# Optimization experiments

Measured on AMD Instinct MI355X. Metric: run time of the kernel, lower is better.

Reference implementation:

```python
import jax, jax.numpy as jnp
import numpy as np

N = 50000          # nodes
E = 400000         # edges
MUL0 = 16          # multiplicity of 0e irreps (node & message)
MUL1 = 8           # multiplicity of 1o irreps
RBF = 8
HID = 64
CUTOFF = 5.0
WNUM = MUL0*MUL0 + MUL1*MUL0 + MUL0*MUL1 + MUL1*MUL1  # 576 tp weights per edge
EPS = 1e-8
INV_SQRT3 = 1.0 / np.sqrt(3.0).astype(np.float32)
A_PATH = 1.0 / np.sqrt(float(MUL0 + MUL1))  # e3nn path normalization (fan_in = 24 for both outputs)


def _split_sv(x):
    # x: [n, 40] -> scalars [n,16], vectors [n,8,3]
    return x[:, :MUL0], x[:, MUL0:].reshape(-1, MUL1, 3)


def _irrep_norm(x):
    # RMS-normalize each irrep block separately (IrrepNorm)
    s, v = _split_sv(x)
    s_rms = jnp.sqrt(jnp.mean(s * s, axis=-1, keepdims=True) + EPS)
    v_rms = jnp.sqrt(jnp.mean(jnp.sum(v * v, axis=-1), axis=-1, keepdims=True) + EPS)
    return jnp.concatenate([s / s_rms, (v / v_rms[:, :, None]).reshape(-1, MUL1 * 3)], axis=-1)


def setup_inputs() -> dict:
    key = jax.random.key(0)
    ks = jax.random.split(key, 20)
    inp = {
        'x': jax.random.normal(ks[0], (N, MUL0 + 3 * MUL1), jnp.float32),
        'edge_src': jax.random.randint(ks[1], (E,), 0, N, jnp.int32),
        'edge_dst': jax.random.randint(ks[2], (E,), 0, N, jnp.int32),
        'edge_sh': jax.random.normal(ks[3], (E, 4), jnp.float32),
        'edge_rbf': jax.random.uniform(ks[4], (E, RBF), jnp.float32),
        'edge_len': jax.random.uniform(ks[5], (E,), jnp.float32) * CUTOFF,
        # radial MLP producing per-edge TP weights
        'w_r1': jax.random.normal(ks[6], (RBF, HID), jnp.float32) / np.sqrt(RBF),
        'b_r1': jnp.zeros((HID,), jnp.float32),
        'w_r2': jax.random.normal(ks[7], (HID, WNUM), jnp.float32) / np.sqrt(HID),
        'b_r2': jnp.zeros((WNUM,), jnp.float32),
        # edge gate MLP
        'w_g1': jax.random.normal(ks[8], (RBF, HID), jnp.float32) / np.sqrt(RBF),
        'b_g1': jnp.zeros((HID,), jnp.float32),
        'w_g2': jax.random.normal(ks[9], (HID, 1), jnp.float32) / np.sqrt(HID),
        'b_g2': jnp.zeros((1,), jnp.float32),
        # msg_linear: 16x0e+8x1o -> (16x0e scalars + 8x0e gates) + 8x1o gated
        'Wm_s': jax.random.normal(ks[10], (MUL0, MUL0 + MUL1), jnp.float32),
        'Wm_v': jax.random.normal(ks[11], (MUL1, MUL1), jnp.float32),
        # update_linear and self_linear: 16x0e+8x1o -> 16x0e+8x1o
        'Wu_s': jax.random.normal(ks[12], (MUL0, MUL0), jnp.float32),
        'Wu_v': jax.random.normal(ks[13], (MUL1, MUL1), jnp.float32),
        'Ws_s': jax.random.normal(ks[14], (MUL0, MUL0), jnp.float32),
        'Ws_v': jax.random.normal(ks[15], (MUL1, MUL1), jnp.float32),
        'res_scale': jnp.asarray(0.1, jnp.float32),
    }
    return inp


def reference(x, edge_src, edge_dst, edge_sh, edge_rbf, edge_len,
              w_r1, b_r1, w_r2, b_r2, w_g1, b_g1, w_g2, b_g2,
              Wm_s, Wm_v, Wu_s, Wu_v, Ws_s, Ws_v, res_scale):
    x_norm = _irrep_norm(x)
    xs, xv = _split_sv(x_norm)

    # per-edge TP weights from radial MLP
    w = jax.nn.silu(edge_rbf @ w_r1 + b_r1) @ w_r2 + b_r2            # [E, 576]
    o = MUL0 * MUL0
    w1 = w[:, :o].reshape(-1, MUL0, MUL0)                            # 0e x 0e -> 0e
    w2 = w[:, o:o + MUL1 * MUL0].reshape(-1, MUL1, MUL0)             # 1o x 1o -> 0e
    o += MUL1 * MUL0
    w3 = w[:, o:o + MUL0 * MUL1].reshape(-1, MUL0, MUL1)             # 0e x 1o -> 1o
    o += MUL0 * MUL1
    w4 = w[:, o:].reshape(-1, MUL1, MUL1)                            # 1o x 0e -> 1o

    # gather per-edge source features
    s_e = xs[edge_src]                                               # [E,16]
    v_e = xv[edge_src]                                               # [E,8,3]
    sh0 = edge_sh[:, :1]                                             # [E,1]
    sh1 = edge_sh[:, 1:4]                                            # [E,3]

    # fully-connected tensor product (CG for l<=1, component norm, path norm)
    m0 = A_PATH * (jnp.einsum('ei,eij->ej', s_e * sh0, w1)
                   + INV_SQRT3 * jnp.einsum('eic,ec,eij->ej', v_e, sh1, w2))   # [E,16]
    m1 = A_PATH * (jnp.einsum('ei,eij,ec->ejc', s_e, w3, sh1)
                   + jnp.einsum('eic,eij->ejc', v_e * sh0[:, :, None], w4))    # [E,8,3]

    # cutoff and sigmoid edge gate
    cw = 0.5 * (jnp.cos(jnp.pi * edge_len / CUTOFF) + 1.0) * (edge_len < CUTOFF)
    gw = jax.nn.sigmoid(jax.nn.silu(edge_rbf @ w_g1 + b_g1) @ w_g2 + b_g2)     # [E,1]
    ew = cw[:, None] * gw                                                      # [E,1]
    m0 = m0 * ew
    m1 = m1 * ew[:, :, None]

    # scatter-add into destination nodes, normalize by total edge weight
    agg0 = jax.ops.segment_sum(m0, edge_dst, num_segments=N)                   # [N,16]
    agg1 = jax.ops.segment_sum(m1.reshape(-1, MUL1 * 3), edge_dst, num_segments=N).reshape(-1, MUL1, 3)
    norm = jax.ops.segment_sum(ew, edge_dst, num_segments=N)                   # [N,1]
    norm = jnp.maximum(norm, EPS)
    agg0 = agg0 / norm
    agg1 = agg1 / norm[:, :, None]

    # msg_linear (equivariant linear, fan-in normalized)
    sc = agg0 @ Wm_s / np.sqrt(MUL0)                                           # [N,24]
    vv = jnp.einsum('nic,ij->njc', agg1, Wm_v) / np.sqrt(MUL1)                 # [N,8,3]

    # gated nonlinearity
    scal = jax.nn.silu(sc[:, :MUL0])
    gates = jax.nn.sigmoid(sc[:, MUL0:])
    vg = vv * gates[:, :, None]

    # update + self interaction, residual
    out_s = scal @ Wu_s / np.sqrt(MUL0) + xs @ Ws_s / np.sqrt(MUL0)
    out_v = (jnp.einsum('nic,ij->njc', vg, Wu_v) + jnp.einsum('nic,ij->njc', xv, Ws_v)) / np.sqrt(MUL1)
    out = jnp.concatenate([out_s, out_v.reshape(-1, MUL1 * 3)], axis=-1)
    return x + res_scale * out
```

## Files before the change

### kernel.cpp

```cpp
#include <hip/hip_runtime.h>
#include <cstdint>

#define MUL0 16
#define MUL1 8
#define NRBF 8
#define HID 64
#define WNUM 576
#define CUTOFF 5.0f
#define EPSF 1e-8f

#define INV_SQRT3 0.57735026918962576f
#define A_PATH    0.20412414523193154f
#define Q16       0.25f
#define Q8        0.35355339059327373f
#define PI_OVER_CUT 0.62831853071795865f

typedef _Float16 f16;
typedef _Float16 f16x8 __attribute__((ext_vector_type(8)));
typedef float f32x4 __attribute__((ext_vector_type(4)));

#define MFMA16(a, b, cc) __builtin_amdgcn_mfma_f32_16x16x32_f16(a, b, cc, 0, 0, 0)

__device__ __forceinline__ float sigm(float x) { return 1.0f / (1.0f + __expf(-x)); }

typedef __attribute__((address_space(1))) const unsigned char* gptr_t;
typedef __attribute__((address_space(3))) unsigned char* lptr_t;

__device__ __forceinline__ void stage16(const void* g, void* l) {
  __builtin_amdgcn_global_load_lds((gptr_t)g, (lptr_t)l, 16, 0, 0);
}

extern "C" __global__ __launch_bounds__(256) void k_prep_w2t(
    const float* __restrict__ w_r2, f16* __restrict__ W2T,
    int* __restrict__ hist, int N) {
  int t = blockIdx.x * 256 + threadIdx.x;
  if (t < HID * WNUM) {
    int n = t >> 6, k = t & 63;
    int jt = n >> 4, cc = n & 15;
    int h = k >> 3, e = k & 7;
    int dst = jt * 1024 + cc * 64 + ((h ^ (cc & 7)) << 3) + e;
    W2T[dst] = (f16)w_r2[k * WNUM + n];
  }
  if (t < N) hist[t] = 0;
}

extern "C" __global__ __launch_bounds__(64) void k_xnorm(
    const float* __restrict__ x, float* __restrict__ xnorm,
    float* __restrict__ agg0, float* __restrict__ agg1,
    float* __restrict__ normb, int N) {
  int n = blockIdx.x * 64 + threadIdx.x;
  if (n >= N) return;
  const float4* xr = (const float4*)(x + (long long)n * 40);
  float4 vv[10];
#pragma unroll
  for (int i = 0; i < 10; i++) vv[i] = xr[i];
  float* f = (float*)vv;
  float ss = 0.f, vs = 0.f;
#pragma unroll
  for (int i = 0; i < 16; i++) ss += f[i] * f[i];
#pragma unroll
  for (int i = 16; i < 40; i++) vs += f[i] * f[i];
  float sr = rsqrtf(ss * (1.0f / 16.0f) + EPSF);
  float vr = rsqrtf(vs * (1.0f / 8.0f) + EPSF);
#pragma unroll
  for (int i = 0; i < 16; i++) f[i] *= sr;
#pragma unroll
  for (int i = 16; i < 40; i++) f[i] *= vr;
  float4* o = (float4*)(xnorm + (long long)n * 40);
#pragma unroll
  for (int i = 0; i < 10; i++) o[i] = vv[i];
  float4 z = {0.f, 0.f, 0.f, 0.f};
  float4* pa0 = (float4*)(agg0 + (long long)n * 16);
#pragma unroll
  for (int i = 0; i < 4; i++) pa0[i] = z;
  float4* pa1 = (float4*)(agg1 + (long long)n * 24);
#pragma unroll
  for (int i = 0; i < 6; i++) pa1[i] = z;
  normb[n] = 0.f;
}

extern "C" __global__ __launch_bounds__(256) void k_hist(
    const int* __restrict__ edst, int* __restrict__ hist, int E) {
  int e = blockIdx.x * 256 + threadIdx.x;
  if (e < E) atomicAdd(&hist[edst[e]], 1);
}

extern "C" __global__ __launch_bounds__(256) void k_scan1(
    const int* __restrict__ hist, int* __restrict__ iscan,
    int* __restrict__ bsum, int N) {
  __shared__ int sm[256];
  int i = blockIdx.x * 256 + threadIdx.x;
  int t = threadIdx.x;
  sm[t] = (i < N) ? hist[i] : 0;
  __syncthreads();
#pragma unroll
  for (int d = 1; d < 256; d <<= 1) {
    int add = (t >= d) ? sm[t - d] : 0;
    __syncthreads();
    sm[t] += add;
    __syncthreads();
  }
  if (i < N) iscan[i] = sm[t];
  if (t == 255) bsum[blockIdx.x] = sm[255];
}

extern "C" __global__ __launch_bounds__(256) void k_scan2(
    int* __restrict__ bsum, int nb) {
  __shared__ int sm[256];
  int t = threadIdx.x;
  sm[t] = (t < nb) ? bsum[t] : 0;
  __syncthreads();
#pragma unroll
  for (int d = 1; d < 256; d <<= 1) {
    int add = (t >= d) ? sm[t - d] : 0;
    __syncthreads();
    sm[t] += add;
    __syncthreads();
  }
  if (t < nb) bsum[t] = sm[t];
}

extern "C" __global__ __launch_bounds__(256) void k_scan3(
    const int* __restrict__ hist, const int* __restrict__ iscan,
    const int* __restrict__ bsum, int* __restrict__ cursor, int N) {
  int i = blockIdx.x * 256 + threadIdx.x;
  if (i >= N) return;
  int base = blockIdx.x ? bsum[blockIdx.x - 1] : 0;
  cursor[i] = iscan[i] - hist[i] + base;
}

extern "C" __global__ __launch_bounds__(256) void k_scatter(
    const int* __restrict__ edst, int* __restrict__ cursor,
    int* __restrict__ perm, int E) {
  int e = blockIdx.x * 256 + threadIdx.x;
  if (e >= E) return;
  int p = atomicAdd(&cursor[edst[e]], 1);
  perm[p] = e;
}

extern "C" __global__ __launch_bounds__(256, 3) void k_edge(
    const float* __restrict__ xnorm, const int* __restrict__ perm,
    const int* __restrict__ esrc, const int* __restrict__ edst,
    const float* __restrict__ sh, const float* __restrict__ rbf,
    const float* __restrict__ elen,
    const float* __restrict__ w_r1, const float* __restrict__ b_r1,
    const float* __restrict__ w_g1, const float* __restrict__ b_g1,
    const float* __restrict__ w_g2, const float* __restrict__ b_g2,
    const float* __restrict__ b_r2, const f16* __restrict__ W2T,
    float* __restrict__ agg0, float* __restrict__ agg1,
    float* __restrict__ normb, int E) {
  __shared__ __align__(16) char smem[53248];
  f16   (*s_H)[32][72]  = (f16(*)[32][72])(smem);
  float (*s_sn)[32][20] = (float(*)[32][20])(smem + 18432);
  float (*s_v)[32][26]  = (float(*)[32][26])(smem + 28672);
  float (*s_a1)[32][10] = (float(*)[32][10])(smem + 41984);
  float (*s_sh)[32][4]  = (float(*)[32][4])(smem + 47104);
  float (*s_rbf)[32][8] = (float(*)[32][8])(smem + 49152);
  float* s_bias = (float*)(smem + 49152);

  const int t = threadIdx.x;
  const int w = t >> 6;
  const int lane = t & 63;
  const long long eb = (long long)blockIdx.x * 128 + w * 32;

  int pl = 0, dstv = 0, srcv = 0;
  float lenv = 1e9f;
  if (lane < 32) {
    long long g2 = eb + lane;
    if (g2 < E) pl = perm[g2];
    srcv = esrc[pl];
    dstv = edst[pl];
    lenv = elen[pl];
    *(float4*)&s_sh[w][lane][0] = *(const float4*)&sh[(long long)pl * 4];
  }
  {
    int e = lane >> 1, half = lane & 1;
    int pe = __shfl(pl, e);
    *(float4*)&s_rbf[w][e][half * 4] =
        *(const float4*)&rbf[(long long)pe * 8 + half * 4];
  }
  __syncthreads();

  {
    const int ge_l = lane >> 2;
    const int part = lane & 3;
#pragma unroll
    for (int g = 0; g < 2; g++) {
      int e = g * 16 + ge_l;
      int srcn = __shfl(srcv, e);
      const float* xr = xnorm + (long long)srcn * 40;
      if (part < 2) {
        float4 aLo = *(const float4*)(xr + part * 8);
        float4 aHi = *(const float4*)(xr + part * 8 + 4);
        *(float4*)&s_sn[w][e][part * 8] = aLo;
        *(float4*)&s_sn[w][e][part * 8 + 4] = aHi;
      } else {
        const int i0 = (part - 2) * 4;
        const float* vp = xr + 16 + i0 * 3;
        float4 v0 = *(const float4*)(vp);
        float4 v1 = *(const float4*)(vp + 4);
        float4 v2 = *(const float4*)(vp + 8);
        *(float4*)&s_v[w][e][i0 * 3] = v0;
        *(float4*)&s_v[w][e][i0 * 3 + 4] = v1;
        *(float4*)&s_v[w][e][i0 * 3 + 8] = v2;
        float4 shq = *(const float4*)&s_sh[w][e][0];
        float s1x = shq.y, s1y = shq.z, s1z = shq.w;
        s_a1[w][e][i0]     = INV_SQRT3 * (v0.x * s1x + v0.y * s1y + v0.z * s1z);
        s_a1[w][e][i0 + 1] = INV_SQRT3 * (v0.w * s1x + v1.x * s1y + v1.y * s1z);
        s_a1[w][e][i0 + 2] = INV_SQRT3 * (v1.z * s1x + v1.w * s1y + v2.x * s1z);
        s_a1[w][e][i0 + 3] = INV_SQRT3 * (v2.y * s1x + v2.z * s1y + v2.w * s1z);
      }
    }
  }

  {
    float wr[8];
#pragma unroll
    for (int r = 0; r < 8; r++) wr[r] = w_r1[r * HID + lane];
    float bh = b_r1[lane];
#pragma unroll 4
    for (int u = 0; u < 32; u++) {
      float4 ra = *(const float4*)&s_rbf[w][u][0];
      float4 rb2 = *(const float4*)&s_rbf[w][u][4];
      float acc = bh + ra.x * wr[0] + ra.y * wr[1] + ra.z * wr[2] + ra.w * wr[3]
                     + rb2.x * wr[4] + rb2.y * wr[5] + rb2.z * wr[6] + rb2.w * wr[7];
      s_H[w][u][lane] = (f16)(acc * sigm(acc));
    }
  }

  float ewv = 0.f;
  {
    const int eg = lane & 31;
    const int hf = lane >> 5;
    float4 ga = *(const float4*)&s_rbf[w][eg][0];
    float4 gb = *(const float4*)&s_rbf[w][eg][4];
    float rv[8] = {ga.x, ga.y, ga.z, ga.w, gb.x, gb.y, gb.z, gb.w};
    float accp = 0.f;
#pragma unroll
    for (int ch = 0; ch < 2; ch++) {
      const int base = hf * 32 + ch * 16;
      float ttv[16];
      {
        const float4 b0 = *(const float4*)&b_g1[base];
        const float4 b1 = *(const float4*)&b_g1[base + 4];
        const float4 b2 = *(const float4*)&b_g1[base + 8];
        const float4 b3 = *(const float4*)&b_g1[base + 12];
        ttv[0] = b0.x; ttv[1] = b0.y; ttv[2] = b0.z; ttv[3] = b0.w;
        ttv[4] = b1.x; ttv[5] = b1.y; ttv[6] = b1.z; ttv[7] = b1.w;
        ttv[8] = b2.x; ttv[9] = b2.y; ttv[10] = b2.z; ttv[11] = b2.w;
        ttv[12] = b3.x; ttv[13] = b3.y; ttv[14] = b3.z; ttv[15] = b3.w;
      }
#pragma unroll
      for (int r = 0; r < 8; r++) {
        const float* wg = w_g1 + r * HID + base;
        float4 w0 = *(const float4*)(wg);
        float4 w1 = *(const float4*)(wg + 4);
        float4 w2 = *(const float4*)(wg + 8);
        float4 w3 = *(const float4*)(wg + 12);
        float rr = rv[r];
        ttv[0] += rr * w0.x; ttv[1] += rr * w0.y; ttv[2] += rr * w0.z; ttv[3] += rr * w0.w;
        ttv[4] += rr * w1.x; ttv[5] += rr * w1.y; ttv[6] += rr * w1.z; ttv[7] += rr * w1.w;
        ttv[8] += rr * w2.x; ttv[9] += rr * w2.y; ttv[10] += rr * w2.z; ttv[11] += rr * w2.w;
        ttv[12] += rr * w3.x; ttv[13] += rr * w3.y; ttv[14] += rr * w3.z; ttv[15] += rr * w3.w;
      }
      const float4 g0 = *(const float4*)&w_g2[base];
      const float4 g1 = *(const float4*)&w_g2[base + 4];
      const float4 g2 = *(const float4*)&w_g2[base + 8];
      const float4 g3 = *(const float4*)&w_g2[base + 12];
      float gw[16] = {g0.x, g0.y, g0.z, g0.w, g1.x, g1.y, g1.z, g1.w,
                      g2.x, g2.y, g2.z, g2.w, g3.x, g3.y, g3.z, g3.w};
#pragma unroll
      for (int k = 0; k < 16; k++) accp += ttv[k] * sigm(ttv[k]) * gw[k];
    }
    accp += __shfl_xor(accp, 32);
    if (lane < 32) {
      long long g2e = eb + lane;
      if (g2e < E) {
        float cw = (lenv < CUTOFF) ? 0.5f * (__cosf(PI_OVER_CUT * lenv) + 1.0f) : 0.f;
        ewv = cw * sigm(accp + b_g2[0]);
      }
    }
  }
  __syncthreads();

  const int quad = lane >> 4;
  const int c = lane & 15;

  const f16x8 af00 = *(const f16x8*)&s_H[w][c][quad * 8];
  const f16x8 af01 = *(const f16x8*)&s_H[w][c][32 + quad * 8];
  const f16x8 af10 = *(const f16x8*)&s_H[w][16 + c][quad * 8];
  const f16x8 af11 = *(const f16x8*)&s_H[w][16 + c][32 + quad * 8];
  for (int i = t; i < WNUM; i += 256) s_bias[i] = b_r2[i];
  __syncthreads();

  char* ring = smem;
  const char* W2Tc = (const char*)W2T;
  const int lofs = w * 1024;
  const int gofs = w * 1024 + lane * 16;

  stage16(W2Tc + gofs, ring + lofs);

  const int rd0 = c * 128 + ((quad ^ (c & 7)) << 4);
  const int rd1 = c * 128 + (((quad + 4) ^ (c & 7)) << 4);

  float p1[2][4] = {{0.f}}, p2[2][4] = {{0.f}}, t3[2][4] = {{0.f}};
  float mx[2][4] = {{0.f}}, my[2][4] = {{0.f}}, mz[2][4] = {{0.f}};

#pragma unroll 1
  for (int ch = 0; ch < 8; ch++) {
    __syncthreads();
    stage16(W2Tc + (ch + 1) * 4096 + gofs, ring + ((ch + 1) & 1) * 4096 + lofs);
    const char* bb = ring + (ch & 1) * 4096;
#pragma unroll
    for (int hf2 = 0; hf2 < 2; hf2++) {
      const int jt = ch * 2 + hf2;
      const char* tb = bb + hf2 * 2048;
      f16x8 b0 = *(const f16x8*)(tb + rd0);
      f16x8 b1 = *(const f16x8*)(tb + rd1);
      float bias = s_bias[jt * 16 + c];
      f32x4 C0 = {0.f, 0.f, 0.f, 0.f};
      C0 = MFMA16(af00, b0, C0); C0 = MFMA16(af01, b1, C0);
      f32x4 C1 = {0.f, 0.f, 0.f, 0.f};
      C1 = MFMA16(af10, b0, C1); C1 = MFMA16(af11, b1, C1);
#pragma unroll
      for (int r = 0; r < 4; r++) {
        p1[0][r] += s_sn[w][quad * 4 + r][jt] * (C0[r] + bias);
        p1[1][r] += s_sn[w][16 + quad * 4 + r][jt] * (C1[r] + bias);
      }
    }
  }
#pragma unroll 1
  for (int ch = 8; ch < 12; ch++) {
    __syncthreads();
    stage16(W2Tc + (ch + 1) * 4096 + gofs, ring + ((ch + 1) & 1) * 4096 + lofs);
    const char* bb = ring + (ch & 1) * 4096;
#pragma unroll
    for (int hf2 = 0; hf2 < 2; hf2++) {
      const int jt = ch * 2 + hf2;
      const char* tb = bb + hf2 * 2048;
      f16x8 b0 = *(const f16x8*)(tb + rd0);
      f16x8 b1 = *(const f16x8*)(tb + rd1);
      float bias = s_bias[jt * 16 + c];
      f32x4 C0 = {0.f, 0.f, 0.f, 0.f};
      C0 = MFMA16(af00, b0, C0); C0 = MFMA16(af01, b1, C0);
      f32x4 C1 = {0.f, 0.f, 0.f, 0.f};
      C1 = MFMA16(af10, b0, C1); C1 = MFMA16(af11, b1, C1);
      const int i = jt - 16;
#pragma unroll
      for (int r = 0; r < 4; r++) {
        p2[0][r] += s_a1[w][quad * 4 + r][i] * (C0[r] + bias);
        p2[1][r] += s_a1[w][16 + quad * 4 + r][i] * (C1[r] + bias);
      }
    }
  }
#pragma unroll 1
  for (int ch = 12; ch < 16; ch++) {
    __syncthreads();
    stage16(W2Tc + (ch + 1) * 4096 + gofs, ring + ((ch + 1) & 1) * 4096 + lofs);
    const char* bb = ring + (ch & 1) * 4096;
#pragma unroll
    for (int hf2 = 0; hf2 < 2; hf2++) {
      const int jt = ch * 2 + hf2;
      const char* tb = bb + hf2 * 2048;
      f16x8 b0 = *(const f16x8*)(tb + rd0);
      f16x8 b1 = *(const f16x8*)(tb + rd1);
      float bias = s_bias[jt * 16 + c];
      f32x4 C0 = {0.f, 0.f, 0.f, 0.f};
      C0 = MFMA16(af00, b0, C0); C0 = MFMA16(af01, b1, C0);
      f32x4 C1 = {0.f, 0.f, 0.f, 0.f};
      C1 = MFMA16(af10, b0, C1); C1 = MFMA16(af11, b1, C1);
      const int i = (jt - 24) * 2 + (c >> 3);
#pragma unroll
      for (int r = 0; r < 4; r++) {
        t3[0][r] += s_sn[w][quad * 4 + r][i] * (C0[r] + bias);
        t3[1][r] += s_sn[w][16 + quad * 4 + r][i] * (C1[r] + bias);
      }
    }
  }
#pragma unroll 1
  for (int ch = 16; ch < 18; ch++) {
    __syncthreads();
    if (ch < 17)
      stage16(W2Tc + (ch + 1) * 4096 + gofs, ring + ((ch + 1) & 1) * 4096 + lofs);
    const char* bb = ring + (ch & 1) * 4096;
#pragma unroll
    for (int hf2 = 0; hf2 < 2; hf2++) {
      const int jt = ch * 2 + hf2;
      const char* tb = bb + hf2 * 2048;
      f16x8 b0 = *(const f16x8*)(tb + rd0);
      f16x8 b1 = *(const f16x8*)(tb + rd1);
      float bias = s_bias[jt * 16 + c];
      f32x4 C0 = {0.f, 0.f, 0.f, 0.f};
      C0 = MFMA16(af00, b0, C0); C0 = MFMA16(af01, b1, C0);
      f32x4 C1 = {0.f, 0.f, 0.f, 0.f};
      C1 = MFMA16(af10, b0, C1); C1 = MFMA16(af11, b1, C1);
      const int i = (jt - 32) * 2 + (c >> 3);
#pragma unroll
      for (int r = 0; r < 4; r++) {
        float wv0 = C0[r] + bias;
        float wv1 = C1[r] + bias;
        mx[0][r] += s_v[w][quad * 4 + r][3 * i] * wv0;
        my[0][r] += s_v[w][quad * 4 + r][3 * i + 1] * wv0;
        mz[0][r] += s_v[w][quad * 4 + r][3 * i + 2] * wv0;
        mx[1][r] += s_v[w][16 + quad * 4 + r][3 * i] * wv1;
        my[1][r] += s_v[w][16 + quad * 4 + r][3 * i + 1] * wv1;
        mz[1][r] += s_v[w][16 + quad * 4 + r][3 * i + 2] * wv1;
      }
    }
  }

#pragma unroll
  for (int g = 0; g < 2; g++)
#pragma unroll
    for (int r = 0; r < 4; r++) {
      t3[g][r] += __shfl_xor(t3[g][r], 8);
      mx[g][r] += __shfl_xor(mx[g][r], 8);
      my[g][r] += __shfl_xor(my[g][r], 8);
      mz[g][r] += __shfl_xor(mz[g][r], 8);
    }

#pragma unroll
  for (int g = 0; g < 2; g++) {
    const int e0g = g * 16 + quad * 4;
    int cur = __shfl(dstv, e0g);
    float acc0 = 0.f, a1x = 0.f, a1y = 0.f, a1z = 0.f, nacc = 0.f;
#pragma unroll
    for (int r = 0; r < 4; r++) {
      const int e = e0g + r;
      const int dst = __shfl(dstv, e);
      const float ew = __shfl(ewv, e);
      if (dst != cur) {
        atomicAdd(&agg0[(long long)cur * 16 + c], acc0);
        if (c < 8) {
          long long b = (long long)cur * 24 + (long long)c * 3;
          atomicAdd(&agg1[b], a1x);
          atomicAdd(&agg1[b + 1], a1y);
          atomicAdd(&agg1[b + 2], a1z);
        } else if (c == 8) {
          atomicAdd(&normb[cur], nacc);
        }
        acc0 = a1x = a1y = a1z = nacc = 0.f;
        cur = dst;
      }
      float sc2 = A_PATH * ew;
      float sh0 = s_sh[w][e][0];
      acc0 += (sh0 * p1[g][r] + p2[g][r]) * sc2;
      if (c < 8) {
        float t3v = t3[g][r] * sc2;
        float scs = sc2 * sh0;
        a1x += t3v * s_sh[w][e][1] + mx[g][r] * scs;
        a1y += t3v * s_sh[w][e][2] + my[g][r] * scs;
        a1z += t3v * s_sh[w][e][3] + mz[g][r] * scs;
      } else if (c == 8) {
        nacc += ew;
      }
    }
    atomicAdd(&agg0[(long long)cur * 16 + c], acc0);
    if (c < 8) {
      long long b = (long long)cur * 24 + (long long)c * 3;
      atomicAdd(&agg1[b], a1x);
      atomicAdd(&agg1[b + 1], a1y);
      atomicAdd(&agg1[b + 2], a1z);
    } else if (c == 8) {
      atomicAdd(&normb[cur], nacc);
    }
  }
}

extern "C" __global__ __launch_bounds__(64) void k_node(
    const float* __restrict__ x, const float* __restrict__ xnorm,
    const float* __restrict__ agg0, const float* __restrict__ agg1,
    const float* __restrict__ normb, const float* __restrict__ Wm_s,
    const float* __restrict__ Wm_v, const float* __restrict__ Wu_s,
    const float* __restrict__ Wu_v, const float* __restrict__ Ws_s,
    const float* __restrict__ Ws_v, const float* __restrict__ res_scale_p,
    float* __restrict__ out, int N) {
  __shared__ float sWms[384];
  __shared__ float sWmv[64];
  __shared__ float sWus[256];
  __shared__ float sWuv[64];
  __shared__ float sWss[256];
  __shared__ float sWsv[64];
  int t = threadIdx.x;
  for (int i = t; i < 384; i += 64) sWms[i] = Wm_s[i];
  sWmv[t] = Wm_v[t];
  for (int i = t; i < 256; i += 64) sWus[i] = Wu_s[i];
  sWuv[t] = Wu_v[t];
  for (int i = t; i < 256; i += 64) sWss[i] = Ws_s[i];
  sWsv[t] = Ws_v[t];
  __syncthreads();
  int n = blockIdx.x * 64 + t;
  if (n >= N) return;

  float inv = 1.0f / fmaxf(normb[n], EPSF);
  float4 a04[4], a14[6];
  {
    const float4* p = (const float4*)(agg0 + (long long)n * 16);
#pragma unroll
    for (int i = 0; i < 4; i++) a04[i] = p[i];
    const float4* q = (const float4*)(agg1 + (long long)n * 24);
#pragma unroll
    for (int i = 0; i < 6; i++) a14[i] = q[i];
  }
  float* a0 = (float*)a04;
  float* a1 = (float*)a14;
#pragma unroll
  for (int i = 0; i < 16; i++) a0[i] *= inv;
#pragma unroll
  for (int i = 0; i < 24; i++) a1[i] *= inv;

  float scal[16], gate[8];
#pragma unroll
  for (int jj = 0; jj < 24; jj++) {
    float acc = 0.f;
#pragma unroll
    for (int i = 0; i < 16; i++) acc += a0[i] * sWms[i * 24 + jj];
    acc *= Q16;
    if (jj < 16) scal[jj] = acc * sigm(acc);
    else gate[jj - 16] = sigm(acc);
  }
  float vg[24];
#pragma unroll
  for (int j = 0; j < 8; j++) {
    float g = gate[j];
#pragma unroll
    for (int cc = 0; cc < 3; cc++) {
      float acc = 0.f;
#pragma unroll
      for (int i = 0; i < 8; i++) acc += a1[i * 3 + cc] * sWmv[i * 8 + j];
      vg[j * 3 + cc] = acc * Q8 * g;
    }
  }
  float4 xn4[10], xo4[10];
  {
    const float4* p = (const float4*)(xnorm + (long long)n * 40);
    const float4* q = (const float4*)(x + (long long)n * 40);
#pragma unroll
    for (int i = 0; i < 10; i++) { xn4[i] = p[i]; xo4[i] = q[i]; }
  }
  const float* xn = (const float*)xn4;
  const float* xo = (const float*)xo4;
  float rs = res_scale_p[0];

  float4 ob[10];
  float* ov = (float*)ob;
#pragma unroll
  for (int j = 0; j < 16; j++) {
    float acc = 0.f, acc2 = 0.f;
#pragma unroll
    for (int i = 0; i < 16; i++) {
      acc += scal[i] * sWus[i * 16 + j];
      acc2 += xn[i] * sWss[i * 16 + j];
    }
    ov[j] = xo[j] + rs * ((acc + acc2) * Q16);
  }
#pragma unroll
  for (int j = 0; j < 8; j++) {
#pragma unroll
    for (int cc = 0; cc < 3; cc++) {
      float acc = 0.f;
#pragma unroll
      for (int i = 0; i < 8; i++)
        acc += vg[i * 3 + cc] * sWuv[i * 8 + j] + xn[16 + i * 3 + cc] * sWsv[i * 8 + j];
      ov[16 + j * 3 + cc] = xo[16 + j * 3 + cc] + rs * (acc * Q8);
    }
  }
  float4* po = (float4*)(out + (long long)n * 40);
#pragma unroll
  for (int i = 0; i < 10; i++) po[i] = ob[i];
}

extern "C" void kernel_launch(void* const* d_in, const int* in_sizes, int n_in,
                              void* d_out, int out_size, void* d_ws, size_t ws_size,
                              hipStream_t stream) {
  const float* x = (const float*)d_in[0];
  const int* esrc = (const int*)d_in[1];
  const int* edst = (const int*)d_in[2];
  const float* sh = (const float*)d_in[3];
  const float* rbf = (const float*)d_in[4];
  const float* elen = (const float*)d_in[5];
  const float* w_r1 = (const float*)d_in[6];
  const float* b_r1 = (const float*)d_in[7];
  const float* w_r2 = (const float*)d_in[8];
  const float* b_r2 = (const float*)d_in[9];
  const float* w_g1 = (const float*)d_in[10];
  const float* b_g1 = (const float*)d_in[11];
  const float* w_g2 = (const float*)d_in[12];
  const float* b_g2 = (const float*)d_in[13];
  const float* Wm_s = (const float*)d_in[14];
  const float* Wm_v = (const float*)d_in[15];
  const float* Wu_s = (const float*)d_in[16];
  const float* Wu_v = (const float*)d_in[17];
  const float* Ws_s = (const float*)d_in[18];
  const float* Ws_v = (const float*)d_in[19];
  const float* res_scale = (const float*)d_in[20];

  const int N = in_sizes[0] / 40;
  const int E = in_sizes[1];

  char* ws = (char*)d_ws;
  size_t off = 0;
  float* xnorm = (float*)(ws + off); off += (size_t)N * 40 * sizeof(float);
  off = (off + 255) & ~(size_t)255;
  float* agg0 = (float*)(ws + off); off += (size_t)N * 16 * sizeof(float);
  float* agg1 = (float*)(ws + off); off += (size_t)N * 24 * sizeof(float);
  float* normb = (float*)(ws + off); off += (size_t)N * sizeof(float);
  off = (off + 255) & ~(size_t)255;
  f16* W2T = (f16*)(ws + off); off += (size_t)WNUM * 64 * sizeof(f16);
  off = (off + 255) & ~(size_t)255;
  int* hist   = (int*)(ws + off); off += (size_t)N * sizeof(int);
  int* iscan  = (int*)(ws + off); off += (size_t)N * sizeof(int);
  int* cursor = (int*)(ws + off); off += (size_t)N * sizeof(int);
  int* bsum   = (int*)(ws + off); off += 256 * sizeof(int);
  off = (off + 255) & ~(size_t)255;
  int* perm   = (int*)(ws + off); off += (size_t)E * sizeof(int);

  const int nbE = (E + 255) / 256;
  const int nbN = (N + 255) / 256;

  k_prep_w2t<<<nbN, 256, 0, stream>>>(w_r2, W2T, hist, N);
  k_hist<<<nbE, 256, 0, stream>>>(edst, hist, E);
  k_scan1<<<nbN, 256, 0, stream>>>(hist, iscan, bsum, N);
  k_scan2<<<1, 256, 0, stream>>>(bsum, nbN);
  k_scan3<<<nbN, 256, 0, stream>>>(hist, iscan, bsum, cursor, N);
  k_scatter<<<nbE, 256, 0, stream>>>(edst, cursor, perm, E);

  k_xnorm<<<(N + 63) / 64, 64, 0, stream>>>(x, xnorm, agg0, agg1, normb, N);

  int nblk = (E + 127) / 128;
  k_edge<<<nblk, 256, 0, stream>>>(xnorm, perm, esrc, edst, sh, rbf, elen,
                                   w_r1, b_r1, w_g1, b_g1, w_g2, b_g2, b_r2,
                                   W2T, agg0, agg1, normb, E);

  k_node<<<(N + 63) / 64, 64, 0, stream>>>(x, xnorm, agg0, agg1, normb, Wm_s,
                                           Wm_v, Wu_s, Wu_v, Ws_s, Ws_v,
                                           res_scale, (float*)d_out, N);
}
```

Baseline: 336.8 us.

## Fuse preprocessing kernels, use single-pass decoupled scan, deepen W2T staging chunks

Merges weight transpose, histogram, and node normalization/zeroing into one kernel and replaces the three-kernel block scan with a single-pass scan, where each block publishes its total and spin-waits on the totals of earlier blocks. The aim is to cut kernel launch count and idle gaps between the small setup kernels. The edge kernel now stages W2T in 8KB chunks of four tiles instead of 4KB chunks of two, halving the number of barriers per edge block. The spin-wait relies on earlier blocks being resident, and the larger staging ring uses more LDS, which could lower occupancy.

```diff
diff --git a/kernel.cpp b/kernel.cpp
--- a/kernel.cpp
+++ b/kernel.cpp
@@ -30,68 +30,65 @@
   __builtin_amdgcn_global_load_lds((gptr_t)g, (lptr_t)l, 16, 0, 0);
 }
 
-extern "C" __global__ __launch_bounds__(256) void k_prep_w2t(
-    const float* __restrict__ w_r2, f16* __restrict__ W2T,
-    int* __restrict__ hist, int N) {
-  int t = blockIdx.x * 256 + threadIdx.x;
-  if (t < HID * WNUM) {
-    int n = t >> 6, k = t & 63;
+extern "C" __global__ __launch_bounds__(256) void k_pre(
+    const float* __restrict__ x, float* __restrict__ xnorm,
+    float* __restrict__ agg0, float* __restrict__ agg1,
+    float* __restrict__ normb, const float* __restrict__ w_r2,
+    f16* __restrict__ W2T, const int* __restrict__ edst,
+    int* __restrict__ hist, int N, int E) {
+  long long gid = (long long)blockIdx.x * 256 + threadIdx.x;
+
+  if (gid < HID * WNUM) {
+    int n = (int)gid >> 6, k = (int)gid & 63;
     int jt = n >> 4, cc = n & 15;
     int h = k >> 3, e = k & 7;
     int dst = jt * 1024 + cc * 64 + ((h ^ (cc & 7)) << 3) + e;
     W2T[dst] = (f16)w_r2[k * WNUM + n];
   }
-  if (t < N) hist[t] = 0;
+
+  if (gid < E) atomicAdd(&hist[edst[gid]], 1);
+
+  if (gid < N) {
+    long long n = gid;
+    const float4* xr = (const float4*)(x + n * 40);
+    float4 vv[10];
+#pragma unroll
+    for (int i = 0; i < 10; i++) vv[i] = xr[i];
+    float* f = (float*)vv;
+    float ss = 0.f, vs = 0.f;
+#pragma unroll
+    for (int i = 0; i < 16; i++) ss += f[i] * f[i];
+#pragma unroll
+    for (int i = 16; i < 40; i++) vs += f[i] * f[i];
+    float sr = rsqrtf(ss * (1.0f / 16.0f) + EPSF);
+    float vr = rsqrtf(vs * (1.0f / 8.0f) + EPSF);
+#pragma unroll
+    for (int i = 0; i < 16; i++) f[i] *= sr;
+#pragma unroll
+    for (int i = 16; i < 40; i++) f[i] *= vr;
+    float4* o = (float4*)(xnorm + n * 40);
+#pragma unroll
+    for (int i = 0; i < 10; i++) o[i] = vv[i];
+    float4 z = {0.f, 0.f, 0.f, 0.f};
+    float4* pa0 = (float4*)(agg0 + n * 16);
+#pragma unroll
+    for (int i = 0; i < 4; i++) pa0[i] = z;
+    float4* pa1 = (float4*)(agg1 + n * 24);
+#pragma unroll
+    for (int i = 0; i < 6; i++) pa1[i] = z;
+    normb[n] = 0.f;
+  }
 }
 
-extern "C" __global__ __launch_bounds__(64) void k_xnorm(
-    const float* __restrict__ x, float* __restrict__ xnorm,
-    float* __restrict__ agg0, float* __restrict__ agg1,
-    float* __restrict__ normb, int N) {
-  int n = blockIdx.x * 64 + threadIdx.x;
-  if (n >= N) return;
-  const float4* xr = (const float4*)(x + (long long)n * 40);
-  float4 vv[10];
-#pragma unroll
-  for (int i = 0; i < 10; i++) vv[i] = xr[i];
-  float* f = (float*)vv;
-  float ss = 0.f, vs = 0.f;
-#pragma unroll
-  for (int i = 0; i < 16; i++) ss += f[i] * f[i];
-#pragma unroll
-  for (int i = 16; i < 40; i++) vs += f[i] * f[i];
-  float sr = rsqrtf(ss * (1.0f / 16.0f) + EPSF);
-  float vr = rsqrtf(vs * (1.0f / 8.0f) + EPSF);
-#pragma unroll
-  for (int i = 0; i < 16; i++) f[i] *= sr;
-#pragma unroll
-  for (int i = 16; i < 40; i++) f[i] *= vr;
-  float4* o = (float4*)(xnorm + (long long)n * 40);
-#pragma unroll
-  for (int i = 0; i < 10; i++) o[i] = vv[i];
-  float4 z = {0.f, 0.f, 0.f, 0.f};
-  float4* pa0 = (float4*)(agg0 + (long long)n * 16);
-#pragma unroll
-  for (int i = 0; i < 4; i++) pa0[i] = z;
-  float4* pa1 = (float4*)(agg1 + (long long)n * 24);
-#pragma unroll
-  for (int i = 0; i < 6; i++) pa1[i] = z;
-  normb[n] = 0.f;
-}
-
-extern "C" __global__ __launch_bounds__(256) void k_hist(
-    const int* __restrict__ edst, int* __restrict__ hist, int E) {
-  int e = blockIdx.x * 256 + threadIdx.x;
-  if (e < E) atomicAdd(&hist[edst[e]], 1);
-}
-
-extern "C" __global__ __launch_bounds__(256) void k_scan1(
-    const int* __restrict__ hist, int* __restrict__ iscan,
-    int* __restrict__ bsum, int N) {
+extern "C" __global__ __launch_bounds__(256) void k_scan(
+    const int* __restrict__ hist, int* __restrict__ cursor,
+    int* __restrict__ pub, int N) {
   __shared__ int sm[256];
-  int i = blockIdx.x * 256 + threadIdx.x;
-  int t = threadIdx.x;
-  sm[t] = (i < N) ? hist[i] : 0;
+  __shared__ int sred[4];
+  const int b = blockIdx.x, t = threadIdx.x;
+  const int i = b * 256 + t;
+  int v = (i < N) ? hist[i] : 0;
+  sm[t] = v;
   __syncthreads();
 #pragma unroll
   for (int d = 1; d < 256; d <<= 1) {
@@ -100,33 +97,26 @@
     sm[t] += add;
     __syncthreads();
   }
-  if (i < N) iscan[i] = sm[t];
-  if (t == 255) bsum[blockIdx.x] = sm[255];
-}
-
-extern "C" __global__ __launch_bounds__(256) void k_scan2(
-    int* __restrict__ bsum, int nb) {
-  __shared__ int sm[256];
-  int t = threadIdx.x;
-  sm[t] = (t < nb) ? bsum[t] : 0;
+  int incl = sm[t];
+  if (t == 255)
+    __hip_atomic_store(&pub[b], sm[255] + 1, __ATOMIC_RELEASE,
+                       __HIP_MEMORY_SCOPE_AGENT);
+  int contrib = 0;
+  if (t < b) {
+    int pv;
+    do {
+      pv = __hip_atomic_load(&pub[t], __ATOMIC_ACQUIRE,
+                             __HIP_MEMORY_SCOPE_AGENT);
+    } while (pv == 0);
+    contrib = pv - 1;
+  }
+#pragma unroll
+  for (int d = 1; d < 64; d <<= 1) contrib += __shfl_xor(contrib, d);
   __syncthreads();
-#pragma unroll
-  for (int d = 1; d < 256; d <<= 1) {
-    int add = (t >= d) ? sm[t - d] : 0;
-    __syncthreads();
-    sm[t] += add;
-    __syncthreads();
-  }
-  if (t < nb) bsum[t] = sm[t];
-}
-
-extern "C" __global__ __launch_bounds__(256) void k_scan3(
-    const int* __restrict__ hist, const int* __restrict__ iscan,
-    const int* __restrict__ bsum, int* __restrict__ cursor, int N) {
-  int i = blockIdx.x * 256 + threadIdx.x;
-  if (i >= N) return;
-  int base = blockIdx.x ? bsum[blockIdx.x - 1] : 0;
-  cursor[i] = iscan[i] - hist[i] + base;
+  if ((t & 63) == 0) sred[t >> 6] = contrib;
+  __syncthreads();
+  int base = sred[0] + sred[1] + sred[2] + sred[3];
+  if (i < N) cursor[i] = base + incl - v;
 }
 
 extern "C" __global__ __launch_bounds__(256) void k_scatter(
@@ -299,6 +289,7 @@
   const int gofs = w * 1024 + lane * 16;
 
   stage16(W2Tc + gofs, ring + lofs);
+  stage16(W2Tc + 4096 + gofs, ring + 4096 + lofs);
 
   const int rd0 = c * 128 + ((quad ^ (c & 7)) << 4);
   const int rd1 = c * 128 + (((quad + 4) ^ (c & 7)) << 4);
@@ -307,14 +298,16 @@
   float mx[2][4] = {{0.f}}, my[2][4] = {{0.f}}, mz[2][4] = {{0.f}};
 
 #pragma unroll 1
-  for (int ch = 0; ch < 8; ch++) {
+  for (int ch = 0; ch < 4; ch++) {
     __syncthreads();
-    stage16(W2Tc + (ch + 1) * 4096 + gofs, ring + ((ch + 1) & 1) * 4096 + lofs);
-    const char* bb = ring + (ch & 1) * 4096;
-#pragma unroll
-    for (int hf2 = 0; hf2 < 2; hf2++) {
-      const int jt = ch * 2 + hf2;
-      const char* tb = bb + hf2 * 2048;
+    stage16(W2Tc + (ch + 1) * 8192 + gofs, ring + ((ch + 1) & 1) * 8192 + lofs);
+    stage16(W2Tc + (ch + 1) * 8192 + 4096 + gofs,
+            ring + ((ch + 1) & 1) * 8192 + 4096 + lofs);
+    const char* bb = ring + (ch & 1) * 8192;
+#pragma unroll
+    for (int q = 0; q < 4; q++) {
+      const int jt = ch * 4 + q;
+      const char* tb = bb + q * 2048;
       f16x8 b0 = *(const f16x8*)(tb + rd0);
       f16x8 b1 = *(const f16x8*)(tb + rd1);
       float bias = s_bias[jt * 16 + c];
@@ -330,14 +323,16 @@
     }
   }
 #pragma unroll 1
-  for (int ch = 8; ch < 12; ch++) {
+  for (int ch = 4; ch < 6; ch++) {
     __syncthreads();
-    stage16(W2Tc + (ch + 1) * 4096 + gofs, ring + ((ch + 1) & 1) * 4096 + lofs);
-    const char* bb = ring + (ch & 1) * 4096;
-#pragma unroll
-    for (int hf2 = 0; hf2 < 2; hf2++) {
-      const int jt = ch * 2 + hf2;
-      const char* tb = bb + hf2 * 2048;
+    stage16(W2Tc + (ch + 1) * 8192 + gofs, ring + ((ch + 1) & 1) * 8192 + lofs);
+    stage16(W2Tc + (ch + 1) * 8192 + 4096 + gofs,
+            ring + ((ch + 1) & 1) * 8192 + 4096 + lofs);
+    const char* bb = ring + (ch & 1) * 8192;
+#pragma unroll
+    for (int q = 0; q < 4; q++) {
+      const int jt = ch * 4 + q;
+      const char* tb = bb + q * 2048;
       f16x8 b0 = *(const f16x8*)(tb + rd0);
       f16x8 b1 = *(const f16x8*)(tb + rd1);
       float bias = s_bias[jt * 16 + c];
@@ -354,14 +349,18 @@
     }
   }
 #pragma unroll 1
-  for (int ch = 12; ch < 16; ch++) {
+  for (int ch = 6; ch < 8; ch++) {
     __syncthreads();
-    stage16(W2Tc + (ch + 1) * 4096 + gofs, ring + ((ch + 1) & 1) * 4096 + lofs);
-    const char* bb = ring + (ch & 1) * 4096;
-#pragma unroll
-    for (int hf2 = 0; hf2 < 2; hf2++) {
-      const int jt = ch * 2 + hf2;
-      const char* tb = bb + hf2 * 2048;
+    if (ch < 8) {
+      stage16(W2Tc + (ch + 1) * 8192 + gofs, ring + ((ch + 1) & 1) * 8192 + lofs);
+      stage16(W2Tc + (ch + 1) * 8192 + 4096 + gofs,
+              ring + ((ch + 1) & 1) * 8192 + 4096 + lofs);
+    }
+    const char* bb = ring + (ch & 1) * 8192;
+#pragma unroll
+    for (int q = 0; q < 4; q++) {
+      const int jt = ch * 4 + q;
+      const char* tb = bb + q * 2048;
       f16x8 b0 = *(const f16x8*)(tb + rd0);
       f16x8 b1 = *(const f16x8*)(tb + rd1);
       float bias = s_bias[jt * 16 + c];
@@ -377,16 +376,13 @@
       }
     }
   }
-#pragma unroll 1
-  for (int ch = 16; ch < 18; ch++) {
+  {
     __syncthreads();
-    if (ch < 17)
-      stage16(W2Tc + (ch + 1) * 4096 + gofs, ring + ((ch + 1) & 1) * 4096 + lofs);
-    const char* bb = ring + (ch & 1) * 4096;
-#pragma unroll
-    for (int hf2 = 0; hf2 < 2; hf2++) {
-      const int jt = ch * 2 + hf2;
-      const char* tb = bb + hf2 * 2048;
+    const char* bb = ring + (8 & 1) * 8192;
+#pragma unroll
+    for (int q = 0; q < 4; q++) {
+      const int jt = 32 + q;
+      const char* tb = bb + q * 2048;
       f16x8 b0 = *(const f16x8*)(tb + rd0);
       f16x8 b1 = *(const f16x8*)(tb + rd1);
       float bias = s_bias[jt * 16 + c];
@@ -394,7 +390,7 @@
       C0 = MFMA16(af00, b0, C0); C0 = MFMA16(af01, b1, C0);
       f32x4 C1 = {0.f, 0.f, 0.f, 0.f};
       C1 = MFMA16(af10, b0, C1); C1 = MFMA16(af11, b1, C1);
-      const int i = (jt - 32) * 2 + (c >> 3);
+      const int i = q * 2 + (c >> 3);
 #pragma unroll
       for (int r = 0; r < 4; r++) {
         float wv0 = C0[r] + bias;
@@ -609,23 +605,20 @@
   f16* W2T = (f16*)(ws + off); off += (size_t)WNUM * 64 * sizeof(f16);
   off = (off + 255) & ~(size_t)255;
   int* hist   = (int*)(ws + off); off += (size_t)N * sizeof(int);
-  int* iscan  = (int*)(ws + off); off += (size_t)N * sizeof(int);
+  int* pub    = (int*)(ws + off); off += 256 * sizeof(int);
   int* cursor = (int*)(ws + off); off += (size_t)N * sizeof(int);
-  int* bsum   = (int*)(ws + off); off += 256 * sizeof(int);
   off = (off + 255) & ~(size_t)255;
   int* perm   = (int*)(ws + off); off += (size_t)E * sizeof(int);
 
   const int nbE = (E + 255) / 256;
   const int nbN = (N + 255) / 256;
 
-  k_prep_w2t<<<nbN, 256, 0, stream>>>(w_r2, W2T, hist, N);
-  k_hist<<<nbE, 256, 0, stream>>>(edst, hist, E);
-  k_scan1<<<nbN, 256, 0, stream>>>(hist, iscan, bsum, N);
-  k_scan2<<<1, 256, 0, stream>>>(bsum, nbN);
-  k_scan3<<<nbN, 256, 0, stream>>>(hist, iscan, bsum, cursor, N);
+  hipMemsetAsync(hist, 0, ((size_t)N + 256) * sizeof(int), stream);
+
+  k_pre<<<nbE, 256, 0, stream>>>(x, xnorm, agg0, agg1, normb, w_r2, W2T,
+                                 edst, hist, N, E);
+  k_scan<<<nbN, 256, 0, stream>>>(hist, cursor, pub, N);
   k_scatter<<<nbE, 256, 0, stream>>>(edst, cursor, perm, E);
-
-  k_xnorm<<<(N + 63) / 64, 64, 0, stream>>>(x, xnorm, agg0, agg1, normb, N);
 
   int nblk = (E + 127) / 128;
   k_edge<<<nblk, 256, 0, stream>>>(xnorm, perm, esrc, edst, sh, rbf, elen,
```

New measurement: 339.7 us. Within noise of the previous version (+0.9%).
